# Kernel tuning notes

Measured on AMD Instinct MI355X. Metric: run time of the kernel, lower is better.

The kernel has to match this reference:

```python
import jax, jax.numpy as jnp
import numpy as np
from jax import lax

HIDDEN = 16
DN = ('NCHW', 'OIHW', 'NCHW')

def setup_inputs() -> dict:
    key = jax.random.key(0)
    k1, k2, k3 = jax.random.split(key, 3)
    b, t, c, h, w = 8, 12, 5, 256, 256
    x = jax.random.normal(k1, (b, t, c, h, w), dtype=jnp.float32)
    # PyTorch-like init scale for conv weights
    W_cell = jax.random.normal(k2, (4 * HIDDEN, c + HIDDEN, 3, 3), dtype=jnp.float32) * 0.05
    b_cell = jnp.zeros((4 * HIDDEN,), dtype=jnp.float32)
    W_final = jax.random.normal(k3, (1, HIDDEN, 1, 1), dtype=jnp.float32) * 0.1
    b_final = jnp.zeros((1,), dtype=jnp.float32)
    return {"x": x, "W_cell": W_cell, "b_cell": b_cell,
            "W_final": W_final, "b_final": b_final}

def _cell_step(h_c, x_t, W_cell, b_cell):
    h_cur, c_cur = h_c
    combined = jnp.concatenate([x_t, h_cur], axis=1)          # [B, C+H, H, W]
    conv = lax.conv_general_dilated(combined, W_cell, (1, 1), 'SAME',
                                    dimension_numbers=DN)
    conv = conv + b_cell[None, :, None, None]                  # [B, 4H, H, W]
    cc_i, cc_f, cc_o, cc_g = jnp.split(conv, 4, axis=1)
    i = jax.nn.sigmoid(cc_i)
    f = jax.nn.sigmoid(cc_f)
    o = jax.nn.sigmoid(cc_o)
    g = jnp.tanh(cc_g)
    c_next = f * c_cur + i * g
    h_next = o * jnp.tanh(c_next)
    return h_next, c_next

def reference(x, W_cell, b_cell, W_final, b_final):
    b, t, c, hh, ww = x.shape
    h0 = jnp.zeros((b, HIDDEN, hh, ww), dtype=x.dtype)
    c0 = jnp.zeros((b, HIDDEN, hh, ww), dtype=x.dtype)
    xt = jnp.moveaxis(x, 1, 0)  # [T, B, C, H, W] for scan over time

    def step(carry, x_t):
        return _cell_step(carry, x_t, W_cell, b_cell), None

    (h_last, _), _ = lax.scan(step, (h0, c0), xt)
    out = lax.conv_general_dilated(h_last, W_final, (1, 1), 'SAME',
                                   dimension_numbers=DN)
    out = out + b_final[None, :, None, None]
    return out
```

## Files before the change

kernel.cpp:

```cpp
#include <hip/hip_runtime.h>
#include <math.h>

#define HIDDEN 16
#define CIN 5
#define BB 8
#define TT 12
#define HH 256
#define WW 256
#define TX 32
#define TY 8
#define HALO_X 34
#define HALO_Y 10
#define NPX (HALO_X * HALO_Y)
#define STRIDE 40

typedef __attribute__((ext_vector_type(8))) short bf16x8;
typedef __attribute__((ext_vector_type(4))) float floatx4;

__device__ __forceinline__ unsigned short f2bf(float f) {
    unsigned int u = __float_as_uint(f);
    u += 0x7fffu + ((u >> 16) & 1u);
    return (unsigned short)(u >> 16);
}
__device__ __forceinline__ float bf2f(unsigned short s) {
    return __uint_as_float(((unsigned int)s) << 16);
}
__device__ __forceinline__ float fast_sigmoid(float x) { return 1.0f / (1.0f + __expf(-x)); }
__device__ __forceinline__ float fast_tanh(float x) {
    float e2 = __expf(-2.0f * fabsf(x));
    float t = (1.0f - e2) / (1.0f + e2);
    return copysignf(t, x);
}

__global__ void prep_w_kernel(const float* __restrict__ Wc,
                              unsigned short* __restrict__ Wfrag) {
    int i = blockIdx.x * 256 + threadIdx.x;
    if (i >= 9 * 4 * 64 * 8) return;
    int j    = i & 7;
    int lane = (i >> 3) & 63;
    int g    = (i >> 9) & 3;
    int tap  = i >> 11;
    int k    = ((lane >> 4) << 3) + j;
    int col  = lane & 15;
    int o    = g * 16 + col;
    float w  = 0.0f;
    if (k < 21) {
        int ci_ref = (k < 16) ? (5 + k) : (k - 16);
        w = Wc[(o * 21 + ci_ref) * 9 + tap];
    }
    Wfrag[i] = f2bf(w);
}

__global__ void prep_x_kernel(const float* __restrict__ x,
                              unsigned short* __restrict__ xp) {
    size_t n = (size_t)blockIdx.x * 256 + threadIdx.x;
    const size_t TOTPX = (size_t)BB * TT * HH * WW;
    if (n >= TOTPX) return;
    size_t bt  = n / (size_t)(HH * WW);
    size_t pix = n - bt * (size_t)(HH * WW);
    const float* src = x + bt * (size_t)CIN * HH * WW + pix;
    unsigned short v[8];
    #pragma unroll
    for (int c = 0; c < CIN; ++c) v[c] = f2bf(src[(size_t)c * HH * WW]);
    v[5] = 0; v[6] = 0; v[7] = 0;
    *(uint4*)&xp[n * 8] = *(const uint4*)v;
}

__global__ __launch_bounds__(256, 5)
void convlstm_step_kernel(const float* __restrict__ x, int t,
                          const unsigned short* __restrict__ xp,
                          const unsigned short* __restrict__ h_in,
                          unsigned short* __restrict__ h_out,
                          float* __restrict__ c_state,
                          const unsigned short* __restrict__ Wfrag,
                          const float* __restrict__ bias,
                          int first, int use_xp) {
    __shared__ unsigned short tile[NPX * STRIDE];

    const int tid  = threadIdx.x;
    const int lane = tid & 63;
    const int wave = tid >> 6;
    const int x0 = blockIdx.x * TX;
    const int y0 = blockIdx.y * TY;
    const int bb = blockIdx.z;

    for (int i = tid; i < NPX; i += 256) {
        int ly = i / HALO_X;
        int lx = i - ly * HALO_X;
        int gy = y0 + ly - 1;
        int gx = x0 + lx - 1;
        bool inb = (gy >= 0 && gy < HH && gx >= 0 && gx < WW);
        unsigned short* row = &tile[i * STRIDE];
        uint4 z = {0, 0, 0, 0};
        if (inb && !first) {
            size_t hb = ((size_t)bb * HH * WW + (size_t)gy * WW + gx) * HIDDEN;
            *(uint4*)&row[0] = *(const uint4*)&h_in[hb];
            *(uint4*)&row[8] = *(const uint4*)&h_in[hb + 8];
        } else {
            *(uint4*)&row[0] = z;
            *(uint4*)&row[8] = z;
        }
        if (use_xp) {
            if (inb) {
                size_t xb = (((size_t)bb * TT + t) * (size_t)(HH * WW)
                             + (size_t)gy * WW + gx) * 8;
                *(uint4*)&row[16] = *(const uint4*)&xp[xb];
            } else {
                *(uint4*)&row[16] = z;
            }
        } else {
            #pragma unroll
            for (int ci = 0; ci < CIN; ++ci) {
                float v = 0.0f;
                if (inb) v = x[(((size_t)bb * TT + t) * CIN + ci) * (size_t)(HH * WW)
                               + (size_t)gy * WW + gx];
                row[16 + ci] = f2bf(v);
            }
            row[21] = 0; row[22] = 0; row[23] = 0;
        }
        *(uint4*)&row[24] = z;
    }
    __syncthreads();

    const int u    = lane & 15;
    const int quad = lane >> 4;

    float bg[4];
    #pragma unroll
    for (int g = 0; g < 4; ++g) bg[g] = bias[g * 16 + u];

    #pragma unroll 1
    for (int half = 0; half < 2; ++half) {
        floatx4 acc[2][4];
        int abase[2];
        #pragma unroll
        for (int mh = 0; mh < 2; ++mh) {
            int ml = half * 2 + mh;
            int m  = wave + ml * 4;
            int my = m >> 1;
            int mx = (m & 1) << 4;
            abase[mh] = (my * HALO_X + mx + u) * STRIDE + quad * 8;
            #pragma unroll
            for (int g = 0; g < 4; ++g)
                acc[mh][g] = (floatx4){bg[g], bg[g], bg[g], bg[g]};
        }

        #pragma unroll 3
        for (int tap = 0; tap < 9; ++tap) {
            int ky = tap / 3;
            int kx = tap - ky * 3;
            int toff = (ky * HALO_X + kx) * STRIDE;
            bf16x8 bfr[4];
            #pragma unroll
            for (int g = 0; g < 4; ++g)
                bfr[g] = *(const bf16x8*)&Wfrag[(size_t)((tap * 4 + g) * 64 + lane) * 8];
            #pragma unroll
            for (int mh = 0; mh < 2; ++mh) {
                bf16x8 af = *(const bf16x8*)&tile[abase[mh] + toff];
                #pragma unroll
                for (int g = 0; g < 4; ++g)
                    acc[mh][g] = __builtin_amdgcn_mfma_f32_16x16x32_bf16(
                        af, bfr[g], acc[mh][g], 0, 0, 0);
            }
        }

        #pragma unroll
        for (int mh = 0; mh < 2; ++mh) {
            int ml = half * 2 + mh;
            int m  = wave + ml * 4;
            int my = m >> 1;
            int mx = (m & 1) << 4;
            int py = y0 + my;
            #pragma unroll
            for (int r = 0; r < 4; ++r) {
                int pxx = x0 + mx + quad * 4 + r;
                size_t idx = ((size_t)bb * HH * WW + (size_t)py * WW + pxx) * HIDDEN + u;
                float ig = fast_sigmoid(acc[mh][0][r]);
                float fg = fast_sigmoid(acc[mh][1][r]);
                float og = fast_sigmoid(acc[mh][2][r]);
                float gg = fast_tanh(acc[mh][3][r]);
                float c_old = first ? 0.0f : c_state[idx];
                float c_new = fg * c_old + ig * gg;
                c_state[idx] = c_new;
                h_out[idx] = f2bf(og * fast_tanh(c_new));
            }
        }
    }
}

__global__ void final_conv_kernel(const unsigned short* __restrict__ h,
                                  const float* __restrict__ Wf,
                                  const float* __restrict__ bf_,
                                  float* __restrict__ out) {
    int i = blockIdx.x * 256 + threadIdx.x;
    if (i >= BB * HH * WW) return;
    size_t base = (size_t)i * HIDDEN;
    uint4 v0 = *(const uint4*)&h[base];
    uint4 v1 = *(const uint4*)&h[base + 8];
    const unsigned short* p0 = (const unsigned short*)&v0;
    const unsigned short* p1 = (const unsigned short*)&v1;
    float s = bf_[0];
    #pragma unroll
    for (int k = 0; k < 8; ++k) s += Wf[k] * bf2f(p0[k]);
    #pragma unroll
    for (int k = 0; k < 8; ++k) s += Wf[8 + k] * bf2f(p1[k]);
    out[i] = s;
}

extern "C" void kernel_launch(void* const* d_in, const int* in_sizes, int n_in,
                              void* d_out, int out_size, void* d_ws, size_t ws_size,
                              hipStream_t stream) {
    const float* x  = (const float*)d_in[0];
    const float* Wc = (const float*)d_in[1];
    const float* bc = (const float*)d_in[2];
    const float* Wf = (const float*)d_in[3];
    const float* bf = (const float*)d_in[4];
    float* out = (float*)d_out;

    char* ws = (char*)d_ws;
    const size_t h_bytes = (size_t)BB * HH * WW * HIDDEN * 2;
    const size_t c_bytes = (size_t)BB * HH * WW * HIDDEN * 4;
    const size_t w_bytes = 9 * 4 * 64 * 8 * 2;
    const size_t x_bytes = (size_t)BB * TT * HH * WW * 8 * 2;

    unsigned short* h_a = (unsigned short*)(ws);
    unsigned short* h_b = (unsigned short*)(ws + h_bytes);
    float* c            = (float*)(ws + 2 * h_bytes);
    unsigned short* Wfr = (unsigned short*)(ws + 2 * h_bytes + c_bytes);
    unsigned short* xp  = (unsigned short*)(ws + 2 * h_bytes + c_bytes + w_bytes);

    const int use_xp =
        (ws_size >= 2 * h_bytes + c_bytes + w_bytes + x_bytes) ? 1 : 0;

    prep_w_kernel<<<(9 * 4 * 64 * 8 + 255) / 256, 256, 0, stream>>>(Wc, Wfr);
    if (use_xp) {
        size_t totpx = (size_t)BB * TT * HH * WW;
        prep_x_kernel<<<(int)((totpx + 255) / 256), 256, 0, stream>>>(x, xp);
    }

    dim3 grid(WW / TX, HH / TY, BB);
    dim3 block(256, 1, 1);

    const unsigned short* h_in = h_a;
    for (int t = 0; t < TT; ++t) {
        unsigned short* h_out = (t & 1) ? h_b : h_a;
        convlstm_step_kernel<<<grid, block, 0, stream>>>(
            x, t, use_xp ? xp : (const unsigned short*)0,
            h_in, h_out, c, Wfr, bc, (t == 0) ? 1 : 0, use_xp);
        h_in = h_out;
    }

    final_conv_kernel<<<(BB * HH * WW + 255) / 256, 256, 0, stream>>>(
        h_in, Wf, bf, out);
}
```

Measured before the change: 691.1 us.

## Fuse all timesteps into one cooperative persistent kernel with register-resident cell state

Replaces the per-timestep launches with a single cooperative kernel of 512 blocks. Each block owns four tiles, keeps their cell state in registers across timesteps, double-buffers the LDS halo staging against the MFMA compute, and uses grid.sync between steps. This removes the fp32 c_state round-trips through global memory and the per-step launch overhead, in exchange for grid-wide barriers, lower occupancy (launch bounds of 2 blocks per CU) and many more live registers. A fallback to per-step launches remains in case the cooperative launch fails, and the final conv now always reads h_b.

```diff
diff --git a/kernel.cpp b/kernel.cpp
--- a/kernel.cpp
+++ b/kernel.cpp
@@ -1,5 +1,8 @@
 #include <hip/hip_runtime.h>
+#include <hip/hip_cooperative_groups.h>
 #include <math.h>
+
+namespace cg = cooperative_groups;
 
 #define HIDDEN 16
 #define CIN 5
@@ -13,6 +16,8 @@
 #define HALO_Y 10
 #define NPX (HALO_X * HALO_Y)
 #define STRIDE 40
+#define NBLK 512
+#define SLOTS 4
 
 typedef __attribute__((ext_vector_type(8))) short bf16x8;
 typedef __attribute__((ext_vector_type(4))) float floatx4;
@@ -66,84 +71,54 @@
     *(uint4*)&xp[n * 8] = *(const uint4*)v;
 }
 
-__global__ __launch_bounds__(256, 5)
-void convlstm_step_kernel(const float* __restrict__ x, int t,
-                          const unsigned short* __restrict__ xp,
-                          const unsigned short* __restrict__ h_in,
-                          unsigned short* __restrict__ h_out,
-                          float* __restrict__ c_state,
-                          const unsigned short* __restrict__ Wfrag,
-                          const float* __restrict__ bias,
-                          int first, int use_xp) {
-    __shared__ unsigned short tile[NPX * STRIDE];
-
-    const int tid  = threadIdx.x;
-    const int lane = tid & 63;
-    const int wave = tid >> 6;
-    const int x0 = blockIdx.x * TX;
-    const int y0 = blockIdx.y * TY;
-    const int bb = blockIdx.z;
-
+__device__ __forceinline__ void stage_tile(unsigned short* __restrict__ dst,
+                                           int tid, int bb, int y0, int x0,
+                                           int t, int first,
+                                           const unsigned short* __restrict__ xp,
+                                           const unsigned short* __restrict__ h_rd) {
     for (int i = tid; i < NPX; i += 256) {
         int ly = i / HALO_X;
         int lx = i - ly * HALO_X;
         int gy = y0 + ly - 1;
         int gx = x0 + lx - 1;
         bool inb = (gy >= 0 && gy < HH && gx >= 0 && gx < WW);
-        unsigned short* row = &tile[i * STRIDE];
+        unsigned short* row = &dst[i * STRIDE];
         uint4 z = {0, 0, 0, 0};
         if (inb && !first) {
             size_t hb = ((size_t)bb * HH * WW + (size_t)gy * WW + gx) * HIDDEN;
-            *(uint4*)&row[0] = *(const uint4*)&h_in[hb];
-            *(uint4*)&row[8] = *(const uint4*)&h_in[hb + 8];
+            *(uint4*)&row[0] = *(const uint4*)&h_rd[hb];
+            *(uint4*)&row[8] = *(const uint4*)&h_rd[hb + 8];
         } else {
             *(uint4*)&row[0] = z;
             *(uint4*)&row[8] = z;
         }
-        if (use_xp) {
-            if (inb) {
-                size_t xb = (((size_t)bb * TT + t) * (size_t)(HH * WW)
-                             + (size_t)gy * WW + gx) * 8;
-                *(uint4*)&row[16] = *(const uint4*)&xp[xb];
-            } else {
-                *(uint4*)&row[16] = z;
-            }
+        if (inb) {
+            size_t xb = (((size_t)bb * TT + t) * (size_t)(HH * WW)
+                         + (size_t)gy * WW + gx) * 8;
+            *(uint4*)&row[16] = *(const uint4*)&xp[xb];
         } else {
-            #pragma unroll
-            for (int ci = 0; ci < CIN; ++ci) {
-                float v = 0.0f;
-                if (inb) v = x[(((size_t)bb * TT + t) * CIN + ci) * (size_t)(HH * WW)
-                               + (size_t)gy * WW + gx];
-                row[16 + ci] = f2bf(v);
-            }
-            row[21] = 0; row[22] = 0; row[23] = 0;
+            *(uint4*)&row[16] = z;
         }
         *(uint4*)&row[24] = z;
     }
-    __syncthreads();
-
-    const int u    = lane & 15;
-    const int quad = lane >> 4;
-
-    float bg[4];
-    #pragma unroll
-    for (int g = 0; g < 4; ++g) bg[g] = bias[g * 16 + u];
-
+}
+
+__device__ __forceinline__ void compute_slot(const unsigned short* __restrict__ buf,
+                                             const unsigned short* __restrict__ Wfrag,
+                                             const float* __restrict__ bg,
+                                             const int* __restrict__ abase,
+                                             int bb, int y0, int x0,
+                                             int lane, int wave, int u, int quad,
+                                             float* __restrict__ creg,
+                                             unsigned short* __restrict__ h_wr) {
     #pragma unroll 1
     for (int half = 0; half < 2; ++half) {
         floatx4 acc[2][4];
-        int abase[2];
-        #pragma unroll
-        for (int mh = 0; mh < 2; ++mh) {
-            int ml = half * 2 + mh;
-            int m  = wave + ml * 4;
-            int my = m >> 1;
-            int mx = (m & 1) << 4;
-            abase[mh] = (my * HALO_X + mx + u) * STRIDE + quad * 8;
+        #pragma unroll
+        for (int mh = 0; mh < 2; ++mh)
             #pragma unroll
             for (int g = 0; g < 4; ++g)
                 acc[mh][g] = (floatx4){bg[g], bg[g], bg[g], bg[g]};
-        }
 
         #pragma unroll 3
         for (int tap = 0; tap < 9; ++tap) {
@@ -156,7 +131,7 @@
                 bfr[g] = *(const bf16x8*)&Wfrag[(size_t)((tap * 4 + g) * 64 + lane) * 8];
             #pragma unroll
             for (int mh = 0; mh < 2; ++mh) {
-                bf16x8 af = *(const bf16x8*)&tile[abase[mh] + toff];
+                bf16x8 af = *(const bf16x8*)&buf[abase[half * 2 + mh] + toff];
                 #pragma unroll
                 for (int g = 0; g < 4; ++g)
                     acc[mh][g] = __builtin_amdgcn_mfma_f32_16x16x32_bf16(
@@ -179,11 +154,148 @@
                 float fg = fast_sigmoid(acc[mh][1][r]);
                 float og = fast_sigmoid(acc[mh][2][r]);
                 float gg = fast_tanh(acc[mh][3][r]);
-                float c_old = first ? 0.0f : c_state[idx];
-                float c_new = fg * c_old + ig * gg;
-                c_state[idx] = c_new;
-                h_out[idx] = f2bf(og * fast_tanh(c_new));
+                float c_new = fg * creg[ml * 4 + r] + ig * gg;
+                creg[ml * 4 + r] = c_new;
+                h_wr[idx] = f2bf(og * fast_tanh(c_new));
             }
+        }
+    }
+}
+
+__global__ __launch_bounds__(256, 2)
+void convlstm_persistent_kernel(const unsigned short* __restrict__ xp,
+                                unsigned short* __restrict__ h_a,
+                                unsigned short* __restrict__ h_b,
+                                const unsigned short* __restrict__ Wfrag,
+                                const float* __restrict__ bias) {
+    cg::grid_group grid = cg::this_grid();
+    __shared__ unsigned short tile[2][NPX * STRIDE];
+
+    const int tid  = threadIdx.x;
+    const int lane = tid & 63;
+    const int wave = tid >> 6;
+    const int u    = lane & 15;
+    const int quad = lane >> 4;
+
+    float bg[4];
+    #pragma unroll
+    for (int g = 0; g < 4; ++g) bg[g] = bias[g * 16 + u];
+
+    int abase[4];
+    #pragma unroll
+    for (int ml = 0; ml < 4; ++ml) {
+        int m  = wave + ml * 4;
+        int my = m >> 1;
+        int mx = (m & 1) << 4;
+        abase[ml] = (my * HALO_X + mx + u) * STRIDE + quad * 8;
+    }
+
+    int sy0[SLOTS], sx0[SLOTS], sbb[SLOTS];
+    #pragma unroll
+    for (int s = 0; s < SLOTS; ++s) {
+        int tileid = (int)blockIdx.x + s * NBLK;
+        sbb[s] = tileid >> 8;
+        int rm = tileid & 255;
+        sy0[s] = (rm >> 3) * TY;
+        sx0[s] = (rm & 7) * TX;
+    }
+
+    float creg[SLOTS][16];
+    #pragma unroll
+    for (int s = 0; s < SLOTS; ++s)
+        #pragma unroll
+        for (int j = 0; j < 16; ++j) creg[s][j] = 0.0f;
+
+    #pragma unroll 1
+    for (int t = 0; t < TT; ++t) {
+        const unsigned short* h_rd = (t & 1) ? h_a : h_b;
+        unsigned short*       h_wr = (t & 1) ? h_b : h_a;
+        const int first = (t == 0);
+
+        stage_tile(tile[0], tid, sbb[0], sy0[0], sx0[0], t, first, xp, h_rd);
+        #pragma unroll 1
+        for (int s = 0; s < SLOTS; ++s) {
+            __syncthreads();
+            if (s < SLOTS - 1)
+                stage_tile(tile[(s + 1) & 1], tid, sbb[s + 1], sy0[s + 1], sx0[s + 1],
+                           t, first, xp, h_rd);
+            compute_slot(tile[s & 1], Wfrag, bg, abase,
+                         sbb[s], sy0[s], sx0[s], lane, wave, u, quad,
+                         creg[s], h_wr);
+        }
+
+        if (t != TT - 1) {
+            __threadfence();
+            grid.sync();
+            __threadfence();
+        }
+    }
+}
+
+__global__ __launch_bounds__(256)
+void convlstm_step_kernel(const unsigned short* __restrict__ xp, int t,
+                          const unsigned short* __restrict__ h_in,
+                          unsigned short* __restrict__ h_out,
+                          float* __restrict__ c_state,
+                          const unsigned short* __restrict__ Wfrag,
+                          const float* __restrict__ bias,
+                          int first) {
+    __shared__ unsigned short tile[NPX * STRIDE];
+
+    const int tid  = threadIdx.x;
+    const int lane = tid & 63;
+    const int wave = tid >> 6;
+    const int u    = lane & 15;
+    const int quad = lane >> 4;
+    const int x0 = blockIdx.x * TX;
+    const int y0 = blockIdx.y * TY;
+    const int bb = blockIdx.z;
+
+    float bg[4];
+    #pragma unroll
+    for (int g = 0; g < 4; ++g) bg[g] = bias[g * 16 + u];
+
+    int abase[4];
+    #pragma unroll
+    for (int ml = 0; ml < 4; ++ml) {
+        int m  = wave + ml * 4;
+        int my = m >> 1;
+        int mx = (m & 1) << 4;
+        abase[ml] = (my * HALO_X + mx + u) * STRIDE + quad * 8;
+    }
+
+    stage_tile(tile, tid, bb, y0, x0, t, first, xp, h_in);
+    __syncthreads();
+
+    float creg[16];
+    #pragma unroll
+    for (int ml = 0; ml < 4; ++ml) {
+        int m  = wave + ml * 4;
+        int my = m >> 1;
+        int mx = (m & 1) << 4;
+        int py = y0 + my;
+        #pragma unroll
+        for (int r = 0; r < 4; ++r) {
+            int pxx = x0 + mx + quad * 4 + r;
+            size_t idx = ((size_t)bb * HH * WW + (size_t)py * WW + pxx) * HIDDEN + u;
+            creg[ml * 4 + r] = first ? 0.0f : c_state[idx];
+        }
+    }
+
+    compute_slot(tile, Wfrag, bg, abase, bb, y0, x0, lane, wave, u, quad,
+                 creg, h_out);
+
+    #pragma unroll
+    for (int ml = 0; ml < 4; ++ml) {
+        int m  = wave + ml * 4;
+        int my = m >> 1;
+        int mx = (m & 1) << 4;
+        int py = y0 + my;
+        #pragma unroll
+        for (int r = 0; r < 4; ++r) {
+            int pxx = x0 + mx + quad * 4 + r;
+            size_t idx = ((size_t)bb * HH * WW + (size_t)py * WW + pxx) * HIDDEN + u;
+            c_state[idx] = creg[ml * 4 + r];
         }
     }
 }
@@ -219,37 +331,39 @@
 
     char* ws = (char*)d_ws;
     const size_t h_bytes = (size_t)BB * HH * WW * HIDDEN * 2;
-    const size_t c_bytes = (size_t)BB * HH * WW * HIDDEN * 4;
-    const size_t w_bytes = 9 * 4 * 64 * 8 * 2;
+    const size_t w_bytes = 64 * 1024;
     const size_t x_bytes = (size_t)BB * TT * HH * WW * 8 * 2;
 
     unsigned short* h_a = (unsigned short*)(ws);
     unsigned short* h_b = (unsigned short*)(ws + h_bytes);
-    float* c            = (float*)(ws + 2 * h_bytes);
-    unsigned short* Wfr = (unsigned short*)(ws + 2 * h_bytes + c_bytes);
-    unsigned short* xp  = (unsigned short*)(ws + 2 * h_bytes + c_bytes + w_bytes);
-
-    const int use_xp =
-        (ws_size >= 2 * h_bytes + c_bytes + w_bytes + x_bytes) ? 1 : 0;
+    unsigned short* Wfr = (unsigned short*)(ws + 2 * h_bytes);
+    unsigned short* xp  = (unsigned short*)(ws + 2 * h_bytes + w_bytes);
+    float* c_fb         = (float*)(ws + 2 * h_bytes + w_bytes + x_bytes);
+    (void)ws_size;
 
     prep_w_kernel<<<(9 * 4 * 64 * 8 + 255) / 256, 256, 0, stream>>>(Wc, Wfr);
-    if (use_xp) {
+    {
         size_t totpx = (size_t)BB * TT * HH * WW;
         prep_x_kernel<<<(int)((totpx + 255) / 256), 256, 0, stream>>>(x, xp);
     }
 
-    dim3 grid(WW / TX, HH / TY, BB);
-    dim3 block(256, 1, 1);
-
-    const unsigned short* h_in = h_a;
-    for (int t = 0; t < TT; ++t) {
-        unsigned short* h_out = (t & 1) ? h_b : h_a;
-        convlstm_step_kernel<<<grid, block, 0, stream>>>(
-            x, t, use_xp ? xp : (const unsigned short*)0,
-            h_in, h_out, c, Wfr, bc, (t == 0) ? 1 : 0, use_xp);
-        h_in = h_out;
+    void* args[] = {(void*)&xp, (void*)&h_a, (void*)&h_b, (void*)&Wfr, (void*)&bc};
+    hipError_t cerr = hipLaunchCooperativeKernel(
+        (void*)convlstm_persistent_kernel, dim3(NBLK), dim3(256), args, 0, stream);
+
+    if (cerr != hipSuccess) {
+        (void)hipGetLastError();
+        dim3 grid(WW / TX, HH / TY, BB);
+        dim3 block(256, 1, 1);
+        const unsigned short* h_in = h_a;
+        for (int t = 0; t < TT; ++t) {
+            unsigned short* h_out = (t & 1) ? h_b : h_a;
+            convlstm_step_kernel<<<grid, block, 0, stream>>>(
+                xp, t, h_in, h_out, c_fb, Wfr, bc, (t == 0) ? 1 : 0);
+            h_in = h_out;
+        }
     }
 
     final_conv_kernel<<<(BB * HH * WW + 255) / 256, 256, 0, stream>>>(
-        h_in, Wf, bf, out);
-}
+        h_b, Wf, bf, out);
+}
```

Result: slower. 2.396 ms (+246.8%).

## Store cell state in MFMA-fragment layout and process all subtiles in one pass

Applied to the files above, without the earlier changes.

Cell state is now kept in a per-tile, per-lane floatx4 layout that matches the MFMA accumulator fragments. It is prefetched before the barrier and written back with vector stores, replacing the scattered scalar loads and stores of c. The two-half loop becomes one fully unrolled pass over all four subtiles per wave, and the fallback path that read x directly is removed. The extra accumulators raise register pressure, so launch bounds drop from 5 to 3 blocks per SM, and the workspace-size check is gone, so the code assumes the workspace is large enough.

```diff
diff --git a/kernel.cpp b/kernel.cpp
--- a/kernel.cpp
+++ b/kernel.cpp
@@ -66,23 +66,27 @@
     *(uint4*)&xp[n * 8] = *(const uint4*)v;
 }
 
-__global__ __launch_bounds__(256, 5)
-void convlstm_step_kernel(const float* __restrict__ x, int t,
-                          const unsigned short* __restrict__ xp,
+__global__ __launch_bounds__(256, 3)
+void convlstm_step_kernel(const unsigned short* __restrict__ xp, int t,
                           const unsigned short* __restrict__ h_in,
                           unsigned short* __restrict__ h_out,
-                          float* __restrict__ c_state,
+                          floatx4* __restrict__ c_ws,
                           const unsigned short* __restrict__ Wfrag,
                           const float* __restrict__ bias,
-                          int first, int use_xp) {
+                          int first) {
     __shared__ unsigned short tile[NPX * STRIDE];
 
     const int tid  = threadIdx.x;
     const int lane = tid & 63;
     const int wave = tid >> 6;
-    const int x0 = blockIdx.x * TX;
-    const int y0 = blockIdx.y * TY;
+    const int u    = lane & 15;
+    const int quad = lane >> 4;
+    const int bx = blockIdx.x;
+    const int by = blockIdx.y;
     const int bb = blockIdx.z;
+    const int x0 = bx * TX;
+    const int y0 = by * TY;
+    const int tileid = (bb * 32 + by) * 8 + bx;
 
     for (int i = tid; i < NPX; i += 256) {
         int ly = i / HALO_X;
@@ -100,92 +104,91 @@
             *(uint4*)&row[0] = z;
             *(uint4*)&row[8] = z;
         }
-        if (use_xp) {
-            if (inb) {
-                size_t xb = (((size_t)bb * TT + t) * (size_t)(HH * WW)
-                             + (size_t)gy * WW + gx) * 8;
-                *(uint4*)&row[16] = *(const uint4*)&xp[xb];
-            } else {
-                *(uint4*)&row[16] = z;
-            }
+        if (inb) {
+            size_t xb = (((size_t)bb * TT + t) * (size_t)(HH * WW)
+                         + (size_t)gy * WW + gx) * 8;
+            *(uint4*)&row[16] = *(const uint4*)&xp[xb];
         } else {
-            #pragma unroll
-            for (int ci = 0; ci < CIN; ++ci) {
-                float v = 0.0f;
-                if (inb) v = x[(((size_t)bb * TT + t) * CIN + ci) * (size_t)(HH * WW)
-                               + (size_t)gy * WW + gx];
-                row[16 + ci] = f2bf(v);
-            }
-            row[21] = 0; row[22] = 0; row[23] = 0;
+            *(uint4*)&row[16] = z;
         }
         *(uint4*)&row[24] = z;
     }
+
+    floatx4 cv[4];
+    const size_t cbase = ((size_t)tileid * 4 + wave) * 64 + lane;
+    if (!first) {
+        #pragma unroll
+        for (int ml = 0; ml < 4; ++ml) cv[ml] = c_ws[cbase * 4 + ml];
+    } else {
+        #pragma unroll
+        for (int ml = 0; ml < 4; ++ml) cv[ml] = (floatx4){0.f, 0.f, 0.f, 0.f};
+    }
+
+    float bg[4];
+    #pragma unroll
+    for (int g = 0; g < 4; ++g) bg[g] = bias[g * 16 + u];
+
+    int abase[4];
+    #pragma unroll
+    for (int ml = 0; ml < 4; ++ml) {
+        int m  = wave + ml * 4;
+        int my = m >> 1;
+        int mx = (m & 1) << 4;
+        abase[ml] = (my * HALO_X + mx + u) * STRIDE + quad * 8;
+    }
+
     __syncthreads();
 
-    const int u    = lane & 15;
-    const int quad = lane >> 4;
-
-    float bg[4];
-    #pragma unroll
-    for (int g = 0; g < 4; ++g) bg[g] = bias[g * 16 + u];
-
-    #pragma unroll 1
-    for (int half = 0; half < 2; ++half) {
-        floatx4 acc[2][4];
-        int abase[2];
-        #pragma unroll
-        for (int mh = 0; mh < 2; ++mh) {
-            int ml = half * 2 + mh;
-            int m  = wave + ml * 4;
-            int my = m >> 1;
-            int mx = (m & 1) << 4;
-            abase[mh] = (my * HALO_X + mx + u) * STRIDE + quad * 8;
+    floatx4 acc[4][4];
+    #pragma unroll
+    for (int ml = 0; ml < 4; ++ml)
+        #pragma unroll
+        for (int g = 0; g < 4; ++g)
+            acc[ml][g] = (floatx4){bg[g], bg[g], bg[g], bg[g]};
+
+    #pragma unroll
+    for (int tap = 0; tap < 9; ++tap) {
+        const int ky = tap / 3;
+        const int kx = tap - ky * 3;
+        const int toff = (ky * HALO_X + kx) * STRIDE;
+        bf16x8 bfr[4];
+        #pragma unroll
+        for (int g = 0; g < 4; ++g)
+            bfr[g] = *(const bf16x8*)&Wfrag[(size_t)((tap * 4 + g) * 64 + lane) * 8];
+        bf16x8 af[4];
+        #pragma unroll
+        for (int ml = 0; ml < 4; ++ml)
+            af[ml] = *(const bf16x8*)&tile[abase[ml] + toff];
+        #pragma unroll
+        for (int ml = 0; ml < 4; ++ml)
             #pragma unroll
             for (int g = 0; g < 4; ++g)
-                acc[mh][g] = (floatx4){bg[g], bg[g], bg[g], bg[g]};
+                acc[ml][g] = __builtin_amdgcn_mfma_f32_16x16x32_bf16(
+                    af[ml], bfr[g], acc[ml][g], 0, 0, 0);
+    }
+
+    #pragma unroll
+    for (int ml = 0; ml < 4; ++ml) {
+        int m  = wave + ml * 4;
+        int my = m >> 1;
+        int mx = (m & 1) << 4;
+        int py = y0 + my;
+        #pragma unroll
+        for (int r = 0; r < 4; ++r) {
+            int pxx = x0 + mx + quad * 4 + r;
+            size_t idx = ((size_t)bb * HH * WW + (size_t)py * WW + pxx) * HIDDEN + u;
+            float ig = fast_sigmoid(acc[ml][0][r]);
+            float fg = fast_sigmoid(acc[ml][1][r]);
+            float og = fast_sigmoid(acc[ml][2][r]);
+            float gg = fast_tanh(acc[ml][3][r]);
+            float c_new = fg * cv[ml][r] + ig * gg;
+            cv[ml][r] = c_new;
+            h_out[idx] = f2bf(og * fast_tanh(c_new));
         }
-
-        #pragma unroll 3
-        for (int tap = 0; tap < 9; ++tap) {
-            int ky = tap / 3;
-            int kx = tap - ky * 3;
-            int toff = (ky * HALO_X + kx) * STRIDE;
-            bf16x8 bfr[4];
-            #pragma unroll
-            for (int g = 0; g < 4; ++g)
-                bfr[g] = *(const bf16x8*)&Wfrag[(size_t)((tap * 4 + g) * 64 + lane) * 8];
-            #pragma unroll
-            for (int mh = 0; mh < 2; ++mh) {
-                bf16x8 af = *(const bf16x8*)&tile[abase[mh] + toff];
-                #pragma unroll
-                for (int g = 0; g < 4; ++g)
-                    acc[mh][g] = __builtin_amdgcn_mfma_f32_16x16x32_bf16(
-                        af, bfr[g], acc[mh][g], 0, 0, 0);
-            }
-        }
-
-        #pragma unroll
-        for (int mh = 0; mh < 2; ++mh) {
-            int ml = half * 2 + mh;
-            int m  = wave + ml * 4;
-            int my = m >> 1;
-            int mx = (m & 1) << 4;
-            int py = y0 + my;
-            #pragma unroll
-            for (int r = 0; r < 4; ++r) {
-                int pxx = x0 + mx + quad * 4 + r;
-                size_t idx = ((size_t)bb * HH * WW + (size_t)py * WW + pxx) * HIDDEN + u;
-                float ig = fast_sigmoid(acc[mh][0][r]);
-                float fg = fast_sigmoid(acc[mh][1][r]);
-                float og = fast_sigmoid(acc[mh][2][r]);
-                float gg = fast_tanh(acc[mh][3][r]);
-                float c_old = first ? 0.0f : c_state[idx];
-                float c_new = fg * c_old + ig * gg;
-                c_state[idx] = c_new;
-                h_out[idx] = f2bf(og * fast_tanh(c_new));
-            }
-        }
-    }
+    }
+
+    #pragma unroll
+    for (int ml = 0; ml < 4; ++ml) c_ws[cbase * 4 + ml] = cv[ml];
 }
 
 __global__ void final_conv_kernel(const unsigned short* __restrict__ h,
@@ -219,21 +222,18 @@
 
     char* ws = (char*)d_ws;
     const size_t h_bytes = (size_t)BB * HH * WW * HIDDEN * 2;
-    const size_t c_bytes = (size_t)BB * HH * WW * HIDDEN * 4;
-    const size_t w_bytes = 9 * 4 * 64 * 8 * 2;
+    const size_t w_bytes = 64 * 1024;
     const size_t x_bytes = (size_t)BB * TT * HH * WW * 8 * 2;
 
     unsigned short* h_a = (unsigned short*)(ws);
     unsigned short* h_b = (unsigned short*)(ws + h_bytes);
-    float* c            = (float*)(ws + 2 * h_bytes);
-    unsigned short* Wfr = (unsigned short*)(ws + 2 * h_bytes + c_bytes);
-    unsigned short* xp  = (unsigned short*)(ws + 2 * h_bytes + c_bytes + w_bytes);
-
-    const int use_xp =
-        (ws_size >= 2 * h_bytes + c_bytes + w_bytes + x_bytes) ? 1 : 0;
+    unsigned short* Wfr = (unsigned short*)(ws + 2 * h_bytes);
+    unsigned short* xp  = (unsigned short*)(ws + 2 * h_bytes + w_bytes);
+    floatx4* c_ws       = (floatx4*)(ws + 2 * h_bytes + w_bytes + x_bytes);
+    (void)ws_size;
 
     prep_w_kernel<<<(9 * 4 * 64 * 8 + 255) / 256, 256, 0, stream>>>(Wc, Wfr);
-    if (use_xp) {
+    {
         size_t totpx = (size_t)BB * TT * HH * WW;
         prep_x_kernel<<<(int)((totpx + 255) / 256), 256, 0, stream>>>(x, xp);
     }
@@ -245,11 +245,10 @@
     for (int t = 0; t < TT; ++t) {
         unsigned short* h_out = (t & 1) ? h_b : h_a;
         convlstm_step_kernel<<<grid, block, 0, stream>>>(
-            x, t, use_xp ? xp : (const unsigned short*)0,
-            h_in, h_out, c, Wfr, bc, (t == 0) ? 1 : 0, use_xp);
+            xp, t, h_in, h_out, c_ws, Wfr, bc, (t == 0) ? 1 : 0);
         h_in = h_out;
     }
 
     final_conv_kernel<<<(BB * HH * WW + 255) / 256, 256, 0, stream>>>(
-        h_in, Wf, bf, out);
-}
+        h_b, Wf, bf, out);
+}
```

Result: slower. 719.4 us (+4.1%).
